# Performance work log

Hardware: AMD Instinct MI355X
Metric: run time of the kernel (lower is better)

The kernel has to match this reference:

```python
import jax, jax.numpy as jnp
import numpy as np

EPS = 1e-6
LAMB = 0.1
ITERS = 3


def setup_inputs() -> dict:
    key = jax.random.key(0)
    k = jax.random.split(key, 6)
    bi, bt, R, W, D = 128, 128, 36, 50, 1024
    return {
        "img_cls": jax.random.normal(k[0], (bi, D), jnp.float32),
        "imgs": jax.random.normal(k[1], (bi, R, D), jnp.float32),
        "cap_cls": jax.random.normal(k[2], (bt, D), jnp.float32),
        "caps": jax.random.normal(k[3], (bt, W, D), jnp.float32),
        "img_lens": jax.random.randint(k[4], (bi,), 1, R + 1, jnp.int32),
        "cap_lens": jax.random.randint(k[5], (bt,), 1, W + 1, jnp.int32),
    }


def _bregman(cost, mask, r, c):
    # P = exp(-cost/lamb) (masked entries have cost=+inf -> P=0), then
    # iterative row/col rescaling toward marginals r, c.
    P = jnp.where(mask, jnp.exp(-cost / LAMB), 0.0)
    P = P / (jnp.sum(P, axis=(-2, -1), keepdims=True) + EPS)
    for _ in range(ITERS):
        u = P.sum(axis=-1) + EPS          # [bi,bt,R]
        P = P * (r / u)[..., None]
        v = P.sum(axis=-2) + EPS          # [bi,bt,W]
        P = P * (c / v)[:, :, None, :]
    return P


def reference(img_cls, imgs, cap_cls, caps, img_lens, cap_lens):
    imgs = imgs + EPS
    caps = caps + EPS
    # prepend cls token
    imgs = jnp.concatenate([img_cls[:, None, :], imgs], axis=1)   # [bi,R+1,D]
    caps = jnp.concatenate([cap_cls[:, None, :], caps], axis=1)   # [bt,W+1,D]
    imgs = imgs / jnp.linalg.norm(imgs, axis=-1, keepdims=True)
    caps = caps / jnp.linalg.norm(caps, axis=-1, keepdims=True)
    # fine-grained cosine sims: [bi, bt, R+1, W+1]
    fg_sims = jnp.einsum("ird,twd->itrw", imgs, caps)
    il = img_lens + 1
    cl = cap_lens + 1
    R1, W1 = imgs.shape[1], caps.shape[1]
    rmask = jnp.arange(R1)[None, :] < il[:, None]   # [bi,R+1]
    wmask = jnp.arange(W1)[None, :] < cl[:, None]   # [bt,W+1]
    mask = rmask[:, None, :, None] & wmask[None, :, None, :]  # [bi,bt,R+1,W+1]
    # _ave_init: uniform marginals over valid rows/cols
    rvalid = mask.any(axis=-1).astype(fg_sims.dtype)  # [bi,bt,R+1]
    cvalid = mask.any(axis=-2).astype(fg_sims.dtype)  # [bi,bt,W+1]
    r = rvalid / rvalid.sum(axis=-1, keepdims=True)
    c = cvalid / cvalid.sum(axis=-1, keepdims=True)
    cost = 1.0 - fg_sims
    tp = _bregman(cost, mask, r, c)
    sims = jnp.sum(fg_sims * tp * mask.astype(fg_sims.dtype), axis=(-2, -1))
    return sims  # [bi, bt]
```

## Files before the change

kernel.cpp:

```cpp
#include <hip/hip_runtime.h>
#include <hip/hip_fp16.h>

#define EPSF 1e-6f

typedef _Float16 f16x8 __attribute__((ext_vector_type(8)));
typedef float f32x4 __attribute__((ext_vector_type(4)));

#define BK 32
#define SMEM_BYTES 40960
#define BUF_BYTES 10240

#define AS1 __attribute__((address_space(1)))
#define AS3 __attribute__((address_space(3)))

#define VM_WAIT(N) asm volatile("s_waitcnt vmcnt(" #N ")" ::: "memory")
#define LGKM0()    asm volatile("s_waitcnt lgkmcnt(0)" ::: "memory")

template <int CTRL>
__device__ __forceinline__ float dpp_add(float x) {
    int y = __builtin_amdgcn_update_dpp(0, __float_as_int(x), CTRL, 0xf, 0xf, true);
    return x + __int_as_float(y);
}

__device__ __forceinline__ float wave_sum_bc(float x) {
    x = dpp_add<0xB1>(x);
    x = dpp_add<0x4E>(x);
    x = dpp_add<0x141>(x);
    x = dpp_add<0x140>(x);
    x = dpp_add<0x142>(x);
    x = dpp_add<0x143>(x);
    return __int_as_float(__builtin_amdgcn_readlane(__float_as_int(x), 63));
}

__global__ __launch_bounds__(256) void norm_kernel(
        const float* __restrict__ img_cls, const float* __restrict__ imgs,
        const float* __restrict__ cap_cls, const float* __restrict__ caps,
        __half* __restrict__ Ah, __half* __restrict__ Bh) {
    __shared__ float red[4];
    const int row = blockIdx.x;
    const int tid = threadIdx.x;

    const float* src = nullptr;
    __half* dsth;
    float eps_add = EPSF;
    if (row < 64 * 80) {
        const int g = row / 80, r = row % 80;
        dsth = Ah + (size_t)row * 1024 + tid * 4;
        int i = -1, rr = 0;
        if (r < 37)      { i = 2 * g;     rr = r; }
        else if (r < 74) { i = 2 * g + 1; rr = r - 37; }
        if (i >= 0) {
            if (rr == 0) { src = img_cls + (size_t)i * 1024; eps_add = 0.0f; }
            else         { src = imgs + ((size_t)i * 36 + (rr - 1)) * 1024; }
        }
    } else {
        const int row2 = row - 64 * 80;
        const int t = row2 >> 6, r = row2 & 63;
        const int n = r >> 4, fr = r & 15;
        const int kt = tid >> 3, q4 = (tid >> 1) & 3, j = (tid & 1) * 4;
        dsth = Bh + ((size_t)(t * 32 + kt) * 4 + n) * 512 + (q4 * 16 + fr) * 8 + j;
        if (r == 0)       { src = cap_cls + (size_t)t * 1024; eps_add = 0.0f; }
        else if (r <= 50) { src = caps + ((size_t)t * 50 + (r - 1)) * 1024; }
    }

    if (src == nullptr) {
        ushort4 z; z.x = z.y = z.z = z.w = 0;
        *reinterpret_cast<ushort4*>(dsth) = z;
        return;
    }

    float4 v = reinterpret_cast<const float4*>(src)[tid];
    v.x += eps_add; v.y += eps_add; v.z += eps_add; v.w += eps_add;
    float ss = v.x * v.x + v.y * v.y + v.z * v.z + v.w * v.w;
    #pragma unroll
    for (int m = 1; m <= 32; m <<= 1) ss += __shfl_xor(ss, m);
    if ((tid & 63) == 0) red[tid >> 6] = ss;
    __syncthreads();
    const float tot = red[0] + red[1] + red[2] + red[3];
    const float rn = 1.0f / sqrtf(tot);

    ushort4 o;
    o.x = __half_as_ushort(__float2half(v.x * rn));
    o.y = __half_as_ushort(__float2half(v.y * rn));
    o.z = __half_as_ushort(__float2half(v.z * rn));
    o.w = __half_as_ushort(__float2half(v.w * rn));
    *reinterpret_cast<ushort4*>(dsth) = o;
}

__device__ __forceinline__ void stage_octA(const __half* __restrict__ Ag,
                                           __half* buf, int kb, int o, size_t lofs) {
    const __half* src = Ag + (size_t)o * 16384 + kb + lofs;
    __builtin_amdgcn_global_load_lds((const AS1 void*)src,
                                     (AS3 void*)(buf + o * 512), 16, 0, 0);
}

__device__ __forceinline__ void stage_A(const __half* __restrict__ Ag,
                                        __half* buf, int kb, int wave, size_t lofs) {
    stage_octA(Ag, buf, kb, wave, lofs);
    stage_octA(Ag, buf, kb, wave + 4, lofs);
    if (wave < 2) stage_octA(Ag, buf, kb, wave + 8, lofs);
}

__device__ __forceinline__ void ds_af(const __half* buf, int wm, int fr, int q4,
                                      f16x8 af[5]) {
    const int soff = ((q4 ^ ((fr >> 1) & 3)) * 8);
    #pragma unroll
    for (int m = 0; m < 5; ++m) {
        const int R = wm * 80 + m * 16 + fr;
        af[m] = *reinterpret_cast<const f16x8*>(buf + R * BK + soff);
    }
}

__device__ __forceinline__ void load_bf(const __half* __restrict__ Bgw, int kt,
                                        f16x8 bf[4]) {
    const __half* p = Bgw + (size_t)kt * 2048;
    #pragma unroll
    for (int n = 0; n < 4; ++n)
        bf[n] = *reinterpret_cast<const f16x8*>(p + n * 512);
}

__device__ __forceinline__ void mfma_cluster(f32x4 acc[5][4], const f16x8 af[5],
                                             const f16x8 bf[4]) {
    __builtin_amdgcn_s_setprio(1);
    #pragma unroll
    for (int m = 0; m < 5; ++m)
        #pragma unroll
        for (int n = 0; n < 4; ++n)
            acc[m][n] = __builtin_amdgcn_mfma_f32_16x16x32_f16(af[m], bf[n], acc[m][n], 0, 0, 0);
    __builtin_amdgcn_s_setprio(0);
}

__global__ __launch_bounds__(256, 3) void fused_kernel(
        const __half* __restrict__ Ah, const __half* __restrict__ Bh,
        const int* __restrict__ img_lens, const int* __restrict__ cap_lens,
        float* __restrict__ out) {
    __shared__ __align__(16) char smem[SMEM_BYTES];
    __half* lds0 = reinterpret_cast<__half*>(smem);
    __half* lds1 = reinterpret_cast<__half*>(smem + BUF_BYTES);
    __half* lds2 = reinterpret_cast<__half*>(smem + 2 * BUF_BYTES);
    __half* lds3 = reinterpret_cast<__half*>(smem + 3 * BUF_BYTES);

    const int idx = blockIdx.x;
    const int xcd = idx & 7;
    const int within = idx >> 3;
    const int bx = within >> 3;
    const int by = xcd * 8 + (within & 7);

    const int tid = threadIdx.x;
    const int wave = tid >> 6;
    const int lane = tid & 63;
    const int wm = wave >> 1, wn = wave & 1;
    const int fr = lane & 15;
    const int q4 = lane >> 4;

    const __half* Ag = Ah + (size_t)bx * 160 * 1024;
    const __half* Bgw = Bh + (size_t)(2 * by + wn) * 65536 + lane * 8;

    const int rsub = lane >> 2;
    const int segsrc = (lane & 3) ^ ((lane >> 3) & 3);
    const size_t lofs = (size_t)rsub * 1024 + (size_t)(segsrc * 8);

    f32x4 acc[5][4];
    #pragma unroll
    for (int m = 0; m < 5; ++m)
        #pragma unroll
        for (int n = 0; n < 4; ++n) {
            f32x4 z = {0.0f, 0.0f, 0.0f, 0.0f};
            acc[m][n] = z;
        }

    f16x8 bfA[4], bfB[4];

    stage_A(Ag, lds0, 0, wave, lofs);
    load_bf(Bgw, 0, bfA);
    stage_A(Ag, lds1, BK, wave, lofs);
    load_bf(Bgw, 1, bfB);
    stage_A(Ag, lds2, 2 * BK, wave, lofs);
    if (wave < 2) { VM_WAIT(10); } else { VM_WAIT(8); }
    __builtin_amdgcn_s_barrier();

    #define GEMM_TILE(KT, RDBUF, STBUF, CUR)                          \
    {                                                                 \
        f16x8 af[5];                                                  \
        ds_af((RDBUF), wm, fr, q4, af);                               \
        mfma_cluster(acc, af, (CUR));                                 \
        load_bf(Bgw, (KT) + 2, (CUR));                                \
        LGKM0();                                                      \
        stage_A(Ag, (STBUF), ((KT) + 3) * BK, wave, lofs);            \
        if (wave < 2) { VM_WAIT(10); } else { VM_WAIT(8); }           \
        __builtin_amdgcn_s_barrier();                                 \
    }

    #pragma unroll 1
    for (int kt = 0; kt < 28; kt += 4) {
        GEMM_TILE(kt,     lds0, lds3, bfA);
        GEMM_TILE(kt + 1, lds1, lds0, bfB);
        GEMM_TILE(kt + 2, lds2, lds1, bfA);
        GEMM_TILE(kt + 3, lds3, lds2, bfB);
    }
    GEMM_TILE(28, lds0, lds3, bfA);
    #undef GEMM_TILE

    {
        f16x8 af[5];
        ds_af(lds1, wm, fr, q4, af);
        mfma_cluster(acc, af, bfB);
        load_bf(Bgw, 31, bfB);
        LGKM0();
        if (wave < 2) { VM_WAIT(7); } else { VM_WAIT(6); }
        __builtin_amdgcn_s_barrier();
    }
    {
        f16x8 af[5];
        ds_af(lds2, wm, fr, q4, af);
        mfma_cluster(acc, af, bfA);
        LGKM0();
        VM_WAIT(4);
        __builtin_amdgcn_s_barrier();
    }
    {
        f16x8 af[5];
        ds_af(lds3, wm, fr, q4, af);
        VM_WAIT(0);
        mfma_cluster(acc, af, bfB);
    }

    __syncthreads();

    float* fg = reinterpret_cast<float*>(smem) + wave * (37 * 64);
    const int orow = q4 * 4;

    #pragma unroll
    for (int p = 0; p < 2; ++p) {
        if (p) {
            LGKM0();
        }
        #pragma unroll
        for (int pm = 0; pm < 3; ++pm) {
            #pragma unroll
            for (int q = 0; q < 4; ++q) {
                const int lrow = (p ? 32 : 0) + pm * 16 + orow + q;
                const int srow = lrow - (p ? 37 : 0);
                const bool ok = p ? (lrow >= 37 && lrow < 74) : (lrow < 37);
                const int sw = ((srow >> 2) & 3) << 4;
                #pragma unroll
                for (int n = 0; n < 4; ++n)
                    if (ok) fg[srow * 64 + ((n * 16 + fr) ^ sw)] = acc[pm + 2 * p][n][q];
            }
        }

        const int i = 4 * bx + 2 * wm + p;
        const int t = 2 * by + wn;
        const int il = img_lens[i] + 1;
        const int cl = cap_lens[t] + 1;
        const bool vcol = lane < cl;

        #define FGR(r_) fg[(r_) * 64 + (lane ^ ((((r_) >> 2) & 3) << 4))]

        float P[37];
        float ts[4] = {0.f, 0.f, 0.f, 0.f};
        #pragma unroll
        for (int r = 0; r < 37; ++r) {
            const float f = FGR(r);
            const bool act = (r < il) && vcol;
            const float pe = act ? __expf((f - 1.0f) * 10.0f) : 0.0f;
            P[r] = pe;
            ts[r & 3] += pe;
        }
        float tot = (ts[0] + ts[1]) + (ts[2] + ts[3]);
        tot = wave_sum_bc(tot);
        const float s0 = __builtin_amdgcn_rcpf(tot + EPSF);
        #pragma unroll
        for (int r = 0; r < 37; ++r) P[r] *= s0;

        const float rmarg = 1.0f / (float)il;
        const float cmarg = 1.0f / (float)cl;
        float csave = 0.0f;
        for (int it = 0; it < 3; ++it) {
            #pragma unroll
            for (int r = 0; r < 37; ++r) {
                const float u = wave_sum_bc(P[r]);
                P[r] *= rmarg * __builtin_amdgcn_rcpf(u + EPSF);
            }
            float vs[4] = {EPSF, 0.f, 0.f, 0.f};
            #pragma unroll
            for (int r = 0; r < 37; ++r) vs[r & 3] += P[r];
            const float v = (vs[0] + vs[1]) + (vs[2] + vs[3]);
            const float cs = vcol ? cmarg * __builtin_amdgcn_rcpf(v) : 0.0f;
            if (it < 2) {
                #pragma unroll
                for (int r = 0; r < 37; ++r) P[r] *= cs;
            } else {
                csave = cs;
            }
        }

        float ls[4] = {0.f, 0.f, 0.f, 0.f};
        #pragma unroll
        for (int r = 0; r < 37; ++r) {
            const float f = FGR(r);
            const float fm = (r < il) ? f : 0.0f;
            ls[r & 3] = fmaf(fm, P[r], ls[r & 3]);
        }
        float local = csave * ((ls[0] + ls[1]) + (ls[2] + ls[3]));
        local = wave_sum_bc(local);
        if (lane == 0) out[i * 128 + t] = local;
        #undef FGR
    }
}

extern "C" void kernel_launch(void* const* d_in, const int* in_sizes, int n_in,
                              void* d_out, int out_size, void* d_ws, size_t ws_size,
                              hipStream_t stream) {
    const float* img_cls  = (const float*)d_in[0];
    const float* imgs     = (const float*)d_in[1];
    const float* cap_cls  = (const float*)d_in[2];
    const float* caps     = (const float*)d_in[3];
    const int*   img_lens = (const int*)d_in[4];
    const int*   cap_lens = (const int*)d_in[5];
    float* out = (float*)d_out;

    __half* Ah = (__half*)d_ws;
    __half* Bh = Ah + (size_t)64 * 80 * 1024;

    norm_kernel<<<64 * 80 + 128 * 64, 256, 0, stream>>>(img_cls, imgs, cap_cls, caps, Ah, Bh);
    fused_kernel<<<2048, 256, 0, stream>>>(Ah, Bh, img_lens, cap_lens, out);
}
```

Measured before the change: 150.3 us.

## Split fused GEMM+Sinkhorn block across 8 waves with halved per-wave N tile

Raises the block from 4 to 8 waves. Each wave now computes 5x2 MFMA tiles instead of 5x4, so the A-staging work per wave drops and fewer accumulator registers are needed. After the GEMM, the accumulators are scattered into a larger shared fg buffer, and each of the 8 waves then runs the Sinkhorn step for one (image, caption) pair, where before each wave looped over two. This aims to expose more wave-level parallelism and latency hiding. In exchange, LDS per block grows to about 74KB, which limits how many blocks fit per CU, and an extra block-wide barrier is added.

Result: faster. 147.2 us (-2.1%).

```diff
diff --git a/kernel.cpp b/kernel.cpp
--- a/kernel.cpp
+++ b/kernel.cpp
@@ -7,7 +7,7 @@
 typedef float f32x4 __attribute__((ext_vector_type(4)));
 
 #define BK 32
-#define SMEM_BYTES 40960
+#define SMEM_BYTES 75776
 #define BUF_BYTES 10240
 
 #define AS1 __attribute__((address_space(1)))
@@ -97,40 +97,38 @@
 __device__ __forceinline__ void stage_A(const __half* __restrict__ Ag,
                                         __half* buf, int kb, int wave, size_t lofs) {
     stage_octA(Ag, buf, kb, wave, lofs);
-    stage_octA(Ag, buf, kb, wave + 4, lofs);
     if (wave < 2) stage_octA(Ag, buf, kb, wave + 8, lofs);
 }
 
-__device__ __forceinline__ void ds_af(const __half* buf, int wm, int fr, int q4,
+__device__ __forceinline__ void ds_af(const __half* buf, int wm2, int fr, int q4,
                                       f16x8 af[5]) {
     const int soff = ((q4 ^ ((fr >> 1) & 3)) * 8);
     #pragma unroll
     for (int m = 0; m < 5; ++m) {
-        const int R = wm * 80 + m * 16 + fr;
+        const int R = wm2 * 80 + m * 16 + fr;
         af[m] = *reinterpret_cast<const f16x8*>(buf + R * BK + soff);
     }
 }
 
 __device__ __forceinline__ void load_bf(const __half* __restrict__ Bgw, int kt,
-                                        f16x8 bf[4]) {
+                                        f16x8 bf[2]) {
     const __half* p = Bgw + (size_t)kt * 2048;
-    #pragma unroll
-    for (int n = 0; n < 4; ++n)
-        bf[n] = *reinterpret_cast<const f16x8*>(p + n * 512);
-}
-
-__device__ __forceinline__ void mfma_cluster(f32x4 acc[5][4], const f16x8 af[5],
-                                             const f16x8 bf[4]) {
+    bf[0] = *reinterpret_cast<const f16x8*>(p);
+    bf[1] = *reinterpret_cast<const f16x8*>(p + 512);
+}
+
+__device__ __forceinline__ void mfma_cluster(f32x4 acc[5][2], const f16x8 af[5],
+                                             const f16x8 bf[2]) {
     __builtin_amdgcn_s_setprio(1);
     #pragma unroll
     for (int m = 0; m < 5; ++m)
         #pragma unroll
-        for (int n = 0; n < 4; ++n)
+        for (int n = 0; n < 2; ++n)
             acc[m][n] = __builtin_amdgcn_mfma_f32_16x16x32_f16(af[m], bf[n], acc[m][n], 0, 0, 0);
     __builtin_amdgcn_s_setprio(0);
 }
 
-__global__ __launch_bounds__(256, 3) void fused_kernel(
+__global__ __launch_bounds__(512, 4) void fused_kernel(
         const __half* __restrict__ Ah, const __half* __restrict__ Bh,
         const int* __restrict__ img_lens, const int* __restrict__ cap_lens,
         float* __restrict__ out) {
@@ -149,45 +147,47 @@
     const int tid = threadIdx.x;
     const int wave = tid >> 6;
     const int lane = tid & 63;
-    const int wm = wave >> 1, wn = wave & 1;
+    const int wm2 = wave >> 2;
+    const int wn2 = wave & 3;
     const int fr = lane & 15;
     const int q4 = lane >> 4;
 
     const __half* Ag = Ah + (size_t)bx * 160 * 1024;
-    const __half* Bgw = Bh + (size_t)(2 * by + wn) * 65536 + lane * 8;
+    const __half* Bgw = Bh + (size_t)(2 * by + (wn2 >> 1)) * 65536
+                           + (size_t)((wn2 & 1) * 2) * 512 + lane * 8;
 
     const int rsub = lane >> 2;
     const int segsrc = (lane & 3) ^ ((lane >> 3) & 3);
     const size_t lofs = (size_t)rsub * 1024 + (size_t)(segsrc * 8);
 
-    f32x4 acc[5][4];
+    f32x4 acc[5][2];
     #pragma unroll
     for (int m = 0; m < 5; ++m)
         #pragma unroll
-        for (int n = 0; n < 4; ++n) {
+        for (int n = 0; n < 2; ++n) {
             f32x4 z = {0.0f, 0.0f, 0.0f, 0.0f};
             acc[m][n] = z;
         }
 
-    f16x8 bfA[4], bfB[4];
+    f16x8 bfA[2], bfB[2];
 
     stage_A(Ag, lds0, 0, wave, lofs);
     load_bf(Bgw, 0, bfA);
     stage_A(Ag, lds1, BK, wave, lofs);
     load_bf(Bgw, 1, bfB);
     stage_A(Ag, lds2, 2 * BK, wave, lofs);
-    if (wave < 2) { VM_WAIT(10); } else { VM_WAIT(8); }
+    if (wave < 2) { VM_WAIT(6); } else { VM_WAIT(4); }
     __builtin_amdgcn_s_barrier();
 
     #define GEMM_TILE(KT, RDBUF, STBUF, CUR)                          \
     {                                                                 \
         f16x8 af[5];                                                  \
-        ds_af((RDBUF), wm, fr, q4, af);                               \
+        ds_af((RDBUF), wm2, fr, q4, af);                              \
         mfma_cluster(acc, af, (CUR));                                 \
         load_bf(Bgw, (KT) + 2, (CUR));                                \
         LGKM0();                                                      \
         stage_A(Ag, (STBUF), ((KT) + 3) * BK, wave, lofs);            \
-        if (wave < 2) { VM_WAIT(10); } else { VM_WAIT(8); }           \
+        if (wave < 2) { VM_WAIT(6); } else { VM_WAIT(4); }            \
         __builtin_amdgcn_s_barrier();                                 \
     }
 
@@ -203,54 +203,58 @@
 
     {
         f16x8 af[5];
-        ds_af(lds1, wm, fr, q4, af);
+        ds_af(lds1, wm2, fr, q4, af);
         mfma_cluster(acc, af, bfB);
         load_bf(Bgw, 31, bfB);
         LGKM0();
-        if (wave < 2) { VM_WAIT(7); } else { VM_WAIT(6); }
+        if (wave < 2) { VM_WAIT(4); } else { VM_WAIT(3); }
         __builtin_amdgcn_s_barrier();
     }
     {
         f16x8 af[5];
-        ds_af(lds2, wm, fr, q4, af);
+        ds_af(lds2, wm2, fr, q4, af);
         mfma_cluster(acc, af, bfA);
         LGKM0();
-        VM_WAIT(4);
+        VM_WAIT(2);
         __builtin_amdgcn_s_barrier();
     }
     {
         f16x8 af[5];
-        ds_af(lds3, wm, fr, q4, af);
+        ds_af(lds3, wm2, fr, q4, af);
         VM_WAIT(0);
         mfma_cluster(acc, af, bfB);
     }
 
     __syncthreads();
 
-    float* fg = reinterpret_cast<float*>(smem) + wave * (37 * 64);
-    const int orow = q4 * 4;
-
-    #pragma unroll
-    for (int p = 0; p < 2; ++p) {
-        if (p) {
-            LGKM0();
-        }
-        #pragma unroll
-        for (int pm = 0; pm < 3; ++pm) {
+    float* fgall = reinterpret_cast<float*>(smem);
+    const int tt = wn2 >> 1;
+    {
+        #pragma unroll
+        for (int m = 0; m < 5; ++m) {
             #pragma unroll
             for (int q = 0; q < 4; ++q) {
-                const int lrow = (p ? 32 : 0) + pm * 16 + orow + q;
-                const int srow = lrow - (p ? 37 : 0);
-                const bool ok = p ? (lrow >= 37 && lrow < 74) : (lrow < 37);
-                const int sw = ((srow >> 2) & 3) << 4;
+                const int Rl = m * 16 + q4 * 4 + q;
+                const int s = (Rl >= 37) ? 1 : 0;
+                const int sr = Rl - 37 * s;
+                const bool valid = (Rl < 74);
+                const int rg = (wm2 * 2 + s) * 2 + tt;
+                const int sw = ((sr >> 2) & 3) << 4;
                 #pragma unroll
-                for (int n = 0; n < 4; ++n)
-                    if (ok) fg[srow * 64 + ((n * 16 + fr) ^ sw)] = acc[pm + 2 * p][n][q];
+                for (int n = 0; n < 2; ++n) {
+                    const int sc = (wn2 & 1) * 32 + n * 16 + fr;
+                    if (valid)
+                        fgall[rg * 2368 + sr * 64 + (sc ^ sw)] = acc[m][n][q];
+                }
             }
         }
-
-        const int i = 4 * bx + 2 * wm + p;
-        const int t = 2 * by + wn;
+    }
+    __syncthreads();
+
+    {
+        float* fg = fgall + wave * 2368;
+        const int i = 4 * bx + (wave >> 1);
+        const int t = 2 * by + (wave & 1);
         const int il = img_lens[i] + 1;
         const int cl = cap_lens[t] + 1;
         const bool vcol = lane < cl;
@@ -324,5 +328,5 @@
     __half* Bh = Ah + (size_t)64 * 80 * 1024;
 
     norm_kernel<<<64 * 80 + 128 * 64, 256, 0, stream>>>(img_cls, imgs, cap_cls, caps, Ah, Bh);
-    fused_kernel<<<2048, 256, 0, stream>>>(Ah, Bh, img_lens, cap_lens, out);
-}
+    fused_kernel<<<2048, 512, 0, stream>>>(Ah, Bh, img_lens, cap_lens, out);
+}
```
